# Optimization experiments

Hardware: AMD Instinct MI355X
Metric: run time of the kernel (lower is better)

## Reference

```python
import jax, jax.numpy as jnp
import numpy as np
import math

B, S, HID, HEADS = 4, 1024, 1024, 16
DH = HID // HEADS


def setup_inputs() -> dict:
    key = jax.random.key(0)
    ks = jax.random.split(key, 16)
    f = lambda k, shape: jax.random.normal(k, shape, dtype=jnp.float32)
    sc = 1.0 / math.sqrt(HID)
    return {
        "q_a": f(ks[0], (B, S, HID)), "k_a": f(ks[1], (B, S, HID)), "v_a": f(ks[2], (B, S, HID)),
        "q_b": f(ks[3], (B, S, HID)), "k_b": f(ks[4], (B, S, HID)), "v_b": f(ks[5], (B, S, HID)),
        "mask": jnp.ones((B, S), dtype=jnp.int32),
        "Wa": f(ks[6], (3, HID, HID)) * sc, "ba": jnp.zeros((3, HID), jnp.float32),
        "Wb": f(ks[7], (3, HID, HID)) * sc, "bb": jnp.zeros((3, HID), jnp.float32),
        "Wo_a": f(ks[8], (HID, HID)) * sc, "bo_a": jnp.zeros((HID,), jnp.float32),
        "Wo_b": f(ks[9], (HID, HID)) * sc, "bo_b": jnp.zeros((HID,), jnp.float32),
    }


def _proj(x, W, b):
    # torch Linear: x @ W.T + b, then split heads -> [B, heads, S, dh]
    y = x @ W.T + b
    return y.reshape(x.shape[0], -1, HEADS, DH).transpose(0, 2, 1, 3)


def reference(q_a, k_a, v_a, q_b, k_b, v_b, mask, Wa, ba, Wb, bb, Wo_a, bo_a, Wo_b, bo_b):
    qa, ka, va = _proj(q_a, Wa[0], ba[0]), _proj(k_a, Wa[1], ba[1]), _proj(v_a, Wa[2], ba[2])
    qb, kb, vb = _proj(q_b, Wb[0], bb[0]), _proj(k_b, Wb[1], bb[1]), _proj(v_b, Wb[2], bb[2])
    scale = 1.0 / math.sqrt(2 * DH)
    # dual-stream score fusion: self + cross terms, all scaled by 1/sqrt(2*dh)
    corr_a = (jnp.einsum('bhqd,bhkd->bhqk', qa, ka) + jnp.einsum('bhqd,bhkd->bhqk', qa, kb)) * scale
    corr_b = (jnp.einsum('bhqd,bhkd->bhqk', qb, kb) + jnp.einsum('bhqd,bhkd->bhqk', qb, ka)) * scale
    m = (mask == 0)[:, None, None, :]  # key-padding mask broadcast over heads & queries
    corr_a = jnp.where(m, -1e9, corr_a)
    corr_b = jnp.where(m, -1e9, corr_b)
    pa = jax.nn.softmax(corr_a, axis=-1)
    pb = jax.nn.softmax(corr_b, axis=-1)
    ha = jnp.einsum('bhqk,bhkd->bhqd', pa, va).transpose(0, 2, 1, 3).reshape(q_a.shape[0], -1, HID)
    hb = jnp.einsum('bhqk,bhkd->bhqd', pb, vb).transpose(0, 2, 1, 3).reshape(q_b.shape[0], -1, HID)
    return (ha @ Wo_a.T + bo_a, hb @ Wo_b.T + bo_b)
```

## Files before the change

### kernel.cpp

```cpp
#include <hip/hip_runtime.h>


typedef __bf16 bf16;
typedef __bf16 bf16x4 __attribute__((ext_vector_type(4)));
typedef __bf16 bf16x8 __attribute__((ext_vector_type(8)));
typedef float  f32x4  __attribute__((ext_vector_type(4)));

#define HID_C   1024
#define S_C     1024
#define B_C     4
#define H_C     16
#define DH_C    64
#define NTOK    4096

__device__ __forceinline__ void gl_lds16(const bf16* g, bf16* l) {
    __builtin_amdgcn_global_load_lds(
        (const __attribute__((address_space(1))) void*)g,
        (__attribute__((address_space(3))) void*)l, 16, 0, 0);
}

struct CvtArgs {
    const float* src[10];
    bf16*        dst[10];
    int          cum[11];
};

__global__ __launch_bounds__(256) void cvt_all(CvtArgs a) {
    int blk = blockIdx.x;
    int seg = 0;
    while (blk >= a.cum[seg + 1]) ++seg;
    int i = ((blk - a.cum[seg]) * 256 + threadIdx.x) * 4;
    f32x4 v = *(const f32x4*)(a.src[seg] + i);
    *(bf16x4*)(a.dst[seg] + i) = __builtin_convertvector(v, bf16x4);
}

struct GemmJob {
    const bf16* A1; const bf16* W1;
    const bf16* A2; const bf16* W2;
    const float* bias1; const float* bias2;
    void* out; int mode; float scale;
};
struct GemmBatch { GemmJob j[5]; };

__global__ __launch_bounds__(256, 3)
void gemm_bt(GemmBatch gb) {
    const GemmJob jb = gb.j[blockIdx.z];
    const int K = HID_C;
    __shared__ bf16 a_lds[128 * 64];
    __shared__ bf16 w_lds[128 * 64];

    const int tid  = threadIdx.x;
    const int wave = tid >> 6, lane = tid & 63;
    const int quad = lane >> 4, l15 = lane & 15;
    const int swz  = l15 & 7;
    const int row0 = blockIdx.x * 128;
    const int col0 = blockIdx.y * 128;
    const int wr = (wave >> 1) * 64;
    const int wc = (wave & 1) * 64;

    f32x4 acc[4][4] = {};

    const int nkb = jb.A2 ? 32 : 16;
    for (int kb = 0; kb < nkb; ++kb) {
        const bf16* A = (kb < 16) ? jb.A1 : jb.A2;
        const bf16* W = (kb < 16) ? jb.W1 : jb.W2;
        const int k0 = (kb & 15) * 64;
        __syncthreads();
        for (int i = 0; i < 4; ++i) {
            int q = tid + i * 256;
            int r = q >> 3, c = q & 7;
            int gch = c ^ (r & 7);
            gl_lds16(A + (size_t)(row0 + r) * K + k0 + gch * 8, a_lds + q * 8);
            gl_lds16(W + (size_t)(col0 + r) * K + k0 + gch * 8, w_lds + q * 8);
        }
        __syncthreads();
        for (int kk = 0; kk < 2; ++kk) {
            const int ch = ((kk * 4 + quad) ^ swz) * 8;
            bf16x8 af[4], bw[4];
            for (int mi = 0; mi < 4; ++mi)
                af[mi] = *(const bf16x8*)(a_lds + (wr + mi * 16 + l15) * 64 + ch);
            for (int ni = 0; ni < 4; ++ni)
                bw[ni] = *(const bf16x8*)(w_lds + (wc + ni * 16 + l15) * 64 + ch);
            for (int mi = 0; mi < 4; ++mi)
                for (int ni = 0; ni < 4; ++ni)
                    acc[mi][ni] = __builtin_amdgcn_mfma_f32_16x16x32_bf16(af[mi], bw[ni], acc[mi][ni], 0, 0, 0);
        }
    }

    for (int mi = 0; mi < 4; ++mi) {
        for (int ni = 0; ni < 4; ++ni) {
            int colg = col0 + wc + ni * 16 + l15;
            float bv = jb.bias1 ? jb.bias1[colg] : 0.f;
            if (jb.bias2) bv += jb.bias2[colg];
            for (int r = 0; r < 4; ++r) {
                int rowg = row0 + wr + mi * 16 + quad * 4 + r;
                float v = (acc[mi][ni][r] + bv) * jb.scale;
                if (jb.mode == 2) {
                    ((float*)jb.out)[(size_t)rowg * HID_C + colg] = v;
                } else {
                    int b = rowg >> 10, s = rowg & 1023;
                    int h = colg >> 6,  d = colg & 63;
                    size_t idx = (jb.mode == 0)
                        ? ((size_t)((b * H_C + h) * S_C + s) * DH_C + d)
                        : ((size_t)((b * H_C + h) * DH_C + d) * S_C + s);
                    ((bf16*)jb.out)[idx] = (bf16)v;
                }
            }
        }
    }
}

__global__ __launch_bounds__(256, 2)
void attn_fused(const bf16* __restrict__ qp_a, const bf16* __restrict__ qp_b,
                const bf16* __restrict__ ksp,
                const bf16* __restrict__ vT_a, const bf16* __restrict__ vT_b,
                const int* __restrict__ mask,
                bf16* __restrict__ ho_a, bf16* __restrict__ ho_b) {
    __shared__ bf16  k_lds[2][128 * 64];
    __shared__ bf16  vT_lds[2][64 * 128];
    __shared__ float madd[1024];
    __shared__ bf16  p_lds[4 * 32 * 40];

    const int tid  = threadIdx.x;
    const int wave = tid >> 6, lane = tid & 63;
    const int quad = lane >> 4, l15 = lane & 15;
    const int swz  = l15 & 7;
    const int bh = blockIdx.x;
    const int b  = bh >> 4, h = bh & 15;
    const int s0 = blockIdx.y * 128;
    const bf16* qp   = blockIdx.z ? qp_b : qp_a;
    const bf16* vTp  = blockIdx.z ? vT_b : vT_a;
    bf16*       hout = blockIdx.z ? ho_b : ho_a;

    {
        int4 mv = *(const int4*)(mask + b * S_C + tid * 4);
        f32x4 md;
        md[0] = mv.x ? 0.f : -1e9f;
        md[1] = mv.y ? 0.f : -1e9f;
        md[2] = mv.z ? 0.f : -1e9f;
        md[3] = mv.w ? 0.f : -1e9f;
        *(f32x4*)(madd + tid * 4) = md;
    }

    bf16x8 qf[2][2];
    for (int qt = 0; qt < 2; ++qt)
        for (int kk = 0; kk < 2; ++kk)
            qf[qt][kk] = *(const bf16x8*)(qp + ((size_t)bh * S_C + s0 + wave * 32 + qt * 16 + l15) * DH_C
                                          + kk * 32 + quad * 8);

    const bf16* kbase0 = ksp + (size_t)bh * S_C * DH_C;
    const bf16* vbase0 = vTp + (size_t)bh * DH_C * S_C;
    auto stage = [&](int kt, int buf) {
        const bf16* kb = kbase0 + kt * 128 * DH_C;
        const bf16* vb = vbase0 + kt * 128;
        for (int i = 0; i < 4; ++i) {
            int q = tid + i * 256;
            int r = q >> 3, c = q & 7;
            gl_lds16(kb + r * DH_C + ((c ^ (r & 7)) * 8), &k_lds[buf][q * 8]);
            int d = q >> 4, c16 = q & 15;
            gl_lds16(vb + (size_t)d * S_C + ((c16 ^ (d & 7)) * 8), &vT_lds[buf][q * 8]);
        }
    };

    float m_i[2] = {-1e30f, -1e30f}, l_i[2] = {0.f, 0.f};
    f32x4 Oacc[2][4] = {};
    bf16* pw = p_lds + wave * (32 * 40);

    stage(0, 0);
    for (int kt = 0; kt < 8; ++kt) {
        const int cur = kt & 1;
        __syncthreads();
        if (kt < 7) stage(kt + 1, 1 - cur);
        const bf16* kl = k_lds[cur];
        const bf16* vl = vT_lds[cur];

        f32x4 sacc[8][2] = {};
        for (int kk = 0; kk < 2; ++kk) {
            const int ch = ((kk * 4 + quad) ^ swz) * 8;
            for (int ct = 0; ct < 8; ++ct) {
                bf16x8 kf = *(const bf16x8*)(kl + (ct * 16 + l15) * 64 + ch);
                sacc[ct][0] = __builtin_amdgcn_mfma_f32_16x16x32_bf16(kf, qf[0][kk], sacc[ct][0], 0, 0, 0);
                sacc[ct][1] = __builtin_amdgcn_mfma_f32_16x16x32_bf16(kf, qf[1][kk], sacc[ct][1], 0, 0, 0);
            }
        }
        for (int ct = 0; ct < 8; ++ct) {
            f32x4 md = *(const f32x4*)(madd + kt * 128 + ct * 16 + quad * 4);
            for (int qt = 0; qt < 2; ++qt)
                for (int r = 0; r < 4; ++r)
                    sacc[ct][qt][r] += md[r];
        }
        float fac[2];
        for (int qt = 0; qt < 2; ++qt) {
            float tm = sacc[0][qt][0];
            for (int ct = 0; ct < 8; ++ct)
                for (int r = 0; r < 4; ++r) tm = fmaxf(tm, sacc[ct][qt][r]);
            tm = fmaxf(tm, __shfl_xor(tm, 16, 64));
            tm = fmaxf(tm, __shfl_xor(tm, 32, 64));
            float mn = fmaxf(m_i[qt], tm);
            fac[qt] = __builtin_amdgcn_exp2f(m_i[qt] - mn);
            m_i[qt] = mn;
            float ts = 0.f;
            for (int ct = 0; ct < 8; ++ct)
                for (int r = 0; r < 4; ++r) {
                    float p = __builtin_amdgcn_exp2f(sacc[ct][qt][r] - mn);
                    sacc[ct][qt][r] = p;
                    ts += p;
                }
            ts += __shfl_xor(ts, 16, 64);
            ts += __shfl_xor(ts, 32, 64);
            l_i[qt] = l_i[qt] * fac[qt] + ts;
            for (int dt = 0; dt < 4; ++dt)
                for (int r = 0; r < 4; ++r) Oacc[qt][dt][r] *= fac[qt];
        }
        for (int c = 0; c < 4; ++c) {
            for (int qt = 0; qt < 2; ++qt)
                for (int half = 0; half < 2; ++half) {
                    bf16x4 pv = __builtin_convertvector(sacc[2 * c + half][qt], bf16x4);
                    *(bf16x4*)(pw + (qt * 16 + l15) * 40 + half * 16 + quad * 4) = pv;
                }
            bf16x8 pf0 = *(const bf16x8*)(pw + l15 * 40 + quad * 8);
            bf16x8 pf1 = *(const bf16x8*)(pw + (16 + l15) * 40 + quad * 8);
            for (int dt = 0; dt < 4; ++dt) {
                bf16x8 vf = *(const bf16x8*)(vl + (dt * 16 + l15) * 128 + ((c * 4 + quad) ^ swz) * 8);
                Oacc[0][dt] = __builtin_amdgcn_mfma_f32_16x16x32_bf16(vf, pf0, Oacc[0][dt], 0, 0, 0);
                Oacc[1][dt] = __builtin_amdgcn_mfma_f32_16x16x32_bf16(vf, pf1, Oacc[1][dt], 0, 0, 0);
            }
        }
    }

    for (int qt = 0; qt < 2; ++qt) {
        float inv = 1.f / l_i[qt];
        int token = s0 + wave * 32 + qt * 16 + l15;
        for (int dt = 0; dt < 4; ++dt) {
            f32x4 o;
            for (int r = 0; r < 4; ++r) o[r] = Oacc[qt][dt][r] * inv;
            bf16x4 ob = __builtin_convertvector(o, bf16x4);
            *(bf16x4*)(hout + (size_t)(b * S_C + token) * HID_C + h * DH_C + dt * 16 + quad * 4) = ob;
        }
    }
}

extern "C" void kernel_launch(void* const* d_in, const int* in_sizes, int n_in,
                              void* d_out, int out_size, void* d_ws, size_t ws_size,
                              hipStream_t stream) {
    const float* q_a  = (const float*)d_in[0];
    const float* k_a  = (const float*)d_in[1];
    const float* v_a  = (const float*)d_in[2];
    const float* q_b  = (const float*)d_in[3];
    const float* k_b  = (const float*)d_in[4];
    const float* v_b  = (const float*)d_in[5];
    const int*   mask = (const int*)  d_in[6];
    const float* Wa   = (const float*)d_in[7];
    const float* ba   = (const float*)d_in[8];
    const float* Wb   = (const float*)d_in[9];
    const float* bb   = (const float*)d_in[10];
    const float* Wo_a = (const float*)d_in[11];
    const float* bo_a = (const float*)d_in[12];
    const float* Wo_b = (const float*)d_in[13];
    const float* bo_b = (const float*)d_in[14];
    float* out = (float*)d_out;

    constexpr size_t ACT = (size_t)NTOK * HID_C;
    constexpr size_t W3  = 3 * (size_t)HID_C * HID_C;
    constexpr size_t W1  = (size_t)HID_C * HID_C;
    const float SC2 = 0.08838834764831845f * 1.4426950408889634f;

    bf16* w = (bf16*)d_ws;
    bf16* bfa[6];
    for (int i = 0; i < 6; ++i) bfa[i] = w + (size_t)i * ACT;
    bf16* bfWa  = w + 6 * ACT;
    bf16* bfWb  = bfWa + W3;
    bf16* bfWoA = bfWb + W3;
    bf16* bfWoB = bfWoA + W1;
    bf16* qa_p  = bfWoB + W1;
    bf16* qb_p  = qa_p + ACT;
    bf16* ks_p  = qb_p + ACT;
    bf16* vTa   = ks_p + ACT;
    bf16* vTb   = vTa + ACT;
    bf16* ha    = vTb + ACT;
    bf16* hb    = ha + ACT;

    CvtArgs ca;
    const float* srcs[10] = {q_a, k_a, v_a, q_b, k_b, v_b, Wa, Wb, Wo_a, Wo_b};
    bf16* dsts[10] = {bfa[0], bfa[1], bfa[2], bfa[3], bfa[4], bfa[5], bfWa, bfWb, bfWoA, bfWoB};
    int nblk[10] = {4096, 4096, 4096, 4096, 4096, 4096, 3072, 3072, 1024, 1024};
    int cum = 0;
    for (int i = 0; i < 10; ++i) { ca.src[i] = srcs[i]; ca.dst[i] = dsts[i]; ca.cum[i] = cum; cum += nblk[i]; }
    ca.cum[10] = cum;
    cvt_all<<<cum, 256, 0, stream>>>(ca);

    GemmBatch g1;
    g1.j[0] = { bfa[1], bfWa + W1,     bfa[4], bfWb + W1, ba + 1024, bb + 1024, ks_p, 0, 1.f  };
    g1.j[1] = { bfa[0], bfWa,          nullptr, nullptr,  ba,        nullptr,   qa_p, 0, SC2 };
    g1.j[2] = { bfa[3], bfWb,          nullptr, nullptr,  bb,        nullptr,   qb_p, 0, SC2 };
    g1.j[3] = { bfa[2], bfWa + 2 * W1, nullptr, nullptr,  ba + 2048, nullptr,   vTa,  1, 1.f  };
    g1.j[4] = { bfa[5], bfWb + 2 * W1, nullptr, nullptr,  bb + 2048, nullptr,   vTb,  1, 1.f  };
    gemm_bt<<<dim3(NTOK / 128, HID_C / 128, 5), 256, 0, stream>>>(g1);

    dim3 ga(B_C * H_C, S_C / 128, 2);
    attn_fused<<<ga, 256, 0, stream>>>(qa_p, qb_p, ks_p, vTa, vTb, mask, ha, hb);

    GemmBatch g2;
    g2.j[0] = { ha, bfWoA, nullptr, nullptr, bo_a, nullptr, (void*)out, 2, 1.f };
    g2.j[1] = { hb, bfWoB, nullptr, nullptr, bo_b, nullptr,
                (void*)(out + (size_t)NTOK * HID_C), 2, 1.f };
    g2.j[2] = g2.j[0]; g2.j[3] = g2.j[0]; g2.j[4] = g2.j[0];
    gemm_bt<<<dim3(NTOK / 128, HID_C / 128, 2), 256, 0, stream>>>(g2);
}
```

Before: 345.6 us.

## Process both attention streams per block to share K tiles; raise GEMM occupancy hint

The attention kernel now handles streams a and b in the same block, so each shared K tile is loaded into LDS once and used for both streams' scores. This halves the grid and removes the z dimension. The V loads are no longer double-buffered: they are issued at the start of each iteration, and two extra barriers per tile are added. Register pressure rises (two sets of Q fragments, accumulators and P tiles), which could lower occupancy or cause spills. Separately, the GEMM launch bound changes from 3 to 4 blocks per CU, which may force the compiler to use fewer registers.

```diff
diff --git a/kernel.cpp b/kernel.cpp
--- a/kernel.cpp
+++ b/kernel.cpp
@@ -42,7 +42,7 @@
 };
 struct GemmBatch { GemmJob j[5]; };
 
-__global__ __launch_bounds__(256, 3)
+__global__ __launch_bounds__(256, 4)
 void gemm_bt(GemmBatch gb) {
     const GemmJob jb = gb.j[blockIdx.z];
     const int K = HID_C;
@@ -117,7 +117,7 @@
                 const int* __restrict__ mask,
                 bf16* __restrict__ ho_a, bf16* __restrict__ ho_b) {
     __shared__ bf16  k_lds[2][128 * 64];
-    __shared__ bf16  vT_lds[2][64 * 128];
+    __shared__ bf16  v_lds[2][64 * 128];
     __shared__ float madd[1024];
     __shared__ bf16  p_lds[4 * 32 * 40];
 
@@ -128,9 +128,10 @@
     const int bh = blockIdx.x;
     const int b  = bh >> 4, h = bh & 15;
     const int s0 = blockIdx.y * 128;
-    const bf16* qp   = blockIdx.z ? qp_b : qp_a;
-    const bf16* vTp  = blockIdx.z ? vT_b : vT_a;
-    bf16*       hout = blockIdx.z ? ho_b : ho_a;
+
+    const bf16* qs[2] = {qp_a, qp_b};
+    const bf16* vs[2] = {vT_a, vT_b};
+    bf16*       hs[2] = {ho_a, ho_b};
 
     {
         int4 mv = *(const int4*)(mask + b * S_C + tid * 4);
@@ -142,102 +143,125 @@
         *(f32x4*)(madd + tid * 4) = md;
     }
 
-    bf16x8 qf[2][2];
-    for (int qt = 0; qt < 2; ++qt)
-        for (int kk = 0; kk < 2; ++kk)
-            qf[qt][kk] = *(const bf16x8*)(qp + ((size_t)bh * S_C + s0 + wave * 32 + qt * 16 + l15) * DH_C
-                                          + kk * 32 + quad * 8);
+    bf16x8 qf[2][2][2];
+    for (int st = 0; st < 2; ++st)
+        for (int qt = 0; qt < 2; ++qt)
+            for (int kk = 0; kk < 2; ++kk)
+                qf[st][qt][kk] = *(const bf16x8*)(qs[st]
+                    + ((size_t)bh * S_C + s0 + wave * 32 + qt * 16 + l15) * DH_C
+                    + kk * 32 + quad * 8);
 
     const bf16* kbase0 = ksp + (size_t)bh * S_C * DH_C;
-    const bf16* vbase0 = vTp + (size_t)bh * DH_C * S_C;
-    auto stage = [&](int kt, int buf) {
-        const bf16* kb = kbase0 + kt * 128 * DH_C;
-        const bf16* vb = vbase0 + kt * 128;
-        for (int i = 0; i < 4; ++i) {
-            int q = tid + i * 256;
-            int r = q >> 3, c = q & 7;
-            gl_lds16(kb + r * DH_C + ((c ^ (r & 7)) * 8), &k_lds[buf][q * 8]);
-            int d = q >> 4, c16 = q & 15;
-            gl_lds16(vb + (size_t)d * S_C + ((c16 ^ (d & 7)) * 8), &vT_lds[buf][q * 8]);
-        }
-    };
-
-    float m_i[2] = {-1e30f, -1e30f}, l_i[2] = {0.f, 0.f};
-    f32x4 Oacc[2][4] = {};
+
+    float m_i[2][2], l_i[2][2];
+    for (int st = 0; st < 2; ++st)
+        for (int qt = 0; qt < 2; ++qt) { m_i[st][qt] = -1e30f; l_i[st][qt] = 0.f; }
+    f32x4  Oacc[2][2][4] = {};
+    bf16x4 pk[2][8][2];
     bf16* pw = p_lds + wave * (32 * 40);
 
-    stage(0, 0);
+    for (int i = 0; i < 4; ++i) {
+        int q = tid + i * 256;
+        int r = q >> 3, c = q & 7;
+        gl_lds16(kbase0 + r * DH_C + ((c ^ (r & 7)) * 8), &k_lds[0][q * 8]);
+    }
+    __syncthreads();
+
     for (int kt = 0; kt < 8; ++kt) {
         const int cur = kt & 1;
+        for (int st = 0; st < 2; ++st) {
+            const bf16* vb = vs[st] + (size_t)bh * DH_C * S_C + kt * 128;
+            for (int i = 0; i < 4; ++i) {
+                int q = tid + i * 256;
+                int d = q >> 4, c16 = q & 15;
+                gl_lds16(vb + (size_t)d * S_C + ((c16 ^ (d & 7)) * 8), &v_lds[st][q * 8]);
+            }
+        }
+        if (kt < 7) {
+            const bf16* kb = kbase0 + (kt + 1) * 128 * DH_C;
+            for (int i = 0; i < 4; ++i) {
+                int q = tid + i * 256;
+                int r = q >> 3, c = q & 7;
+                gl_lds16(kb + r * DH_C + ((c ^ (r & 7)) * 8), &k_lds[1 - cur][q * 8]);
+            }
+        }
+        const bf16* kl = k_lds[cur];
+
+        for (int st = 0; st < 2; ++st) {
+            f32x4 sacc[8][2] = {};
+            for (int kk = 0; kk < 2; ++kk) {
+                const int ch = ((kk * 4 + quad) ^ swz) * 8;
+                for (int ct = 0; ct < 8; ++ct) {
+                    bf16x8 kf = *(const bf16x8*)(kl + (ct * 16 + l15) * 64 + ch);
+                    sacc[ct][0] = __builtin_amdgcn_mfma_f32_16x16x32_bf16(kf, qf[st][0][kk], sacc[ct][0], 0, 0, 0);
+                    sacc[ct][1] = __builtin_amdgcn_mfma_f32_16x16x32_bf16(kf, qf[st][1][kk], sacc[ct][1], 0, 0, 0);
+                }
+            }
+            for (int ct = 0; ct < 8; ++ct) {
+                f32x4 md = *(const f32x4*)(madd + kt * 128 + ct * 16 + quad * 4);
+                for (int qt = 0; qt < 2; ++qt)
+                    for (int r = 0; r < 4; ++r)
+                        sacc[ct][qt][r] += md[r];
+            }
+            for (int qt = 0; qt < 2; ++qt) {
+                float tm = sacc[0][qt][0];
+                for (int ct = 0; ct < 8; ++ct)
+                    for (int r = 0; r < 4; ++r) tm = fmaxf(tm, sacc[ct][qt][r]);
+                tm = fmaxf(tm, __shfl_xor(tm, 16, 64));
+                tm = fmaxf(tm, __shfl_xor(tm, 32, 64));
+                float mn = fmaxf(m_i[st][qt], tm);
+                float fac = __builtin_amdgcn_exp2f(m_i[st][qt] - mn);
+                m_i[st][qt] = mn;
+                float ts = 0.f;
+                for (int ct = 0; ct < 8; ++ct)
+                    for (int r = 0; r < 4; ++r) {
+                        float p = __builtin_amdgcn_exp2f(sacc[ct][qt][r] - mn);
+                        sacc[ct][qt][r] = p;
+                        ts += p;
+                    }
+                ts += __shfl_xor(ts, 16, 64);
+                ts += __shfl_xor(ts, 32, 64);
+                l_i[st][qt] = l_i[st][qt] * fac + ts;
+                for (int dt = 0; dt < 4; ++dt)
+                    for (int r = 0; r < 4; ++r) Oacc[st][qt][dt][r] *= fac;
+                for (int ct = 0; ct < 8; ++ct)
+                    pk[st][ct][qt] = __builtin_convertvector(sacc[ct][qt], bf16x4);
+            }
+        }
+
         __syncthreads();
-        if (kt < 7) stage(kt + 1, 1 - cur);
-        const bf16* kl = k_lds[cur];
-        const bf16* vl = vT_lds[cur];
-
-        f32x4 sacc[8][2] = {};
-        for (int kk = 0; kk < 2; ++kk) {
-            const int ch = ((kk * 4 + quad) ^ swz) * 8;
-            for (int ct = 0; ct < 8; ++ct) {
-                bf16x8 kf = *(const bf16x8*)(kl + (ct * 16 + l15) * 64 + ch);
-                sacc[ct][0] = __builtin_amdgcn_mfma_f32_16x16x32_bf16(kf, qf[0][kk], sacc[ct][0], 0, 0, 0);
-                sacc[ct][1] = __builtin_amdgcn_mfma_f32_16x16x32_bf16(kf, qf[1][kk], sacc[ct][1], 0, 0, 0);
-            }
-        }
-        for (int ct = 0; ct < 8; ++ct) {
-            f32x4 md = *(const f32x4*)(madd + kt * 128 + ct * 16 + quad * 4);
-            for (int qt = 0; qt < 2; ++qt)
-                for (int r = 0; r < 4; ++r)
-                    sacc[ct][qt][r] += md[r];
-        }
-        float fac[2];
+
+        for (int st = 0; st < 2; ++st) {
+            const bf16* vl = v_lds[st];
+            for (int c = 0; c < 4; ++c) {
+                for (int qt = 0; qt < 2; ++qt)
+                    for (int half = 0; half < 2; ++half)
+                        *(bf16x4*)(pw + (qt * 16 + l15) * 40 + half * 16 + quad * 4)
+                            = pk[st][2 * c + half][qt];
+                bf16x8 pf0 = *(const bf16x8*)(pw + l15 * 40 + quad * 8);
+                bf16x8 pf1 = *(const bf16x8*)(pw + (16 + l15) * 40 + quad * 8);
+                for (int dt = 0; dt < 4; ++dt) {
+                    bf16x8 vf = *(const bf16x8*)(vl + (dt * 16 + l15) * 128 + ((c * 4 + quad) ^ swz) * 8);
+                    Oacc[st][0][dt] = __builtin_amdgcn_mfma_f32_16x16x32_bf16(vf, pf0, Oacc[st][0][dt], 0, 0, 0);
+                    Oacc[st][1][dt] = __builtin_amdgcn_mfma_f32_16x16x32_bf16(vf, pf1, Oacc[st][1][dt], 0, 0, 0);
+                }
+            }
+        }
+
+        __syncthreads();
+    }
+
+    for (int st = 0; st < 2; ++st)
         for (int qt = 0; qt < 2; ++qt) {
-            float tm = sacc[0][qt][0];
-            for (int ct = 0; ct < 8; ++ct)
-                for (int r = 0; r < 4; ++r) tm = fmaxf(tm, sacc[ct][qt][r]);
-            tm = fmaxf(tm, __shfl_xor(tm, 16, 64));
-            tm = fmaxf(tm, __shfl_xor(tm, 32, 64));
-            float mn = fmaxf(m_i[qt], tm);
-            fac[qt] = __builtin_amdgcn_exp2f(m_i[qt] - mn);
-            m_i[qt] = mn;
-            float ts = 0.f;
-            for (int ct = 0; ct < 8; ++ct)
-                for (int r = 0; r < 4; ++r) {
-                    float p = __builtin_amdgcn_exp2f(sacc[ct][qt][r] - mn);
-                    sacc[ct][qt][r] = p;
-                    ts += p;
-                }
-            ts += __shfl_xor(ts, 16, 64);
-            ts += __shfl_xor(ts, 32, 64);
-            l_i[qt] = l_i[qt] * fac[qt] + ts;
-            for (int dt = 0; dt < 4; ++dt)
-                for (int r = 0; r < 4; ++r) Oacc[qt][dt][r] *= fac[qt];
-        }
-        for (int c = 0; c < 4; ++c) {
-            for (int qt = 0; qt < 2; ++qt)
-                for (int half = 0; half < 2; ++half) {
-                    bf16x4 pv = __builtin_convertvector(sacc[2 * c + half][qt], bf16x4);
-                    *(bf16x4*)(pw + (qt * 16 + l15) * 40 + half * 16 + quad * 4) = pv;
-                }
-            bf16x8 pf0 = *(const bf16x8*)(pw + l15 * 40 + quad * 8);
-            bf16x8 pf1 = *(const bf16x8*)(pw + (16 + l15) * 40 + quad * 8);
+            float inv = 1.f / l_i[st][qt];
+            int token = s0 + wave * 32 + qt * 16 + l15;
             for (int dt = 0; dt < 4; ++dt) {
-                bf16x8 vf = *(const bf16x8*)(vl + (dt * 16 + l15) * 128 + ((c * 4 + quad) ^ swz) * 8);
-                Oacc[0][dt] = __builtin_amdgcn_mfma_f32_16x16x32_bf16(vf, pf0, Oacc[0][dt], 0, 0, 0);
-                Oacc[1][dt] = __builtin_amdgcn_mfma_f32_16x16x32_bf16(vf, pf1, Oacc[1][dt], 0, 0, 0);
-            }
-        }
-    }
-
-    for (int qt = 0; qt < 2; ++qt) {
-        float inv = 1.f / l_i[qt];
-        int token = s0 + wave * 32 + qt * 16 + l15;
-        for (int dt = 0; dt < 4; ++dt) {
-            f32x4 o;
-            for (int r = 0; r < 4; ++r) o[r] = Oacc[qt][dt][r] * inv;
-            bf16x4 ob = __builtin_convertvector(o, bf16x4);
-            *(bf16x4*)(hout + (size_t)(b * S_C + token) * HID_C + h * DH_C + dt * 16 + quad * 4) = ob;
-        }
-    }
+                f32x4 o;
+                for (int r = 0; r < 4; ++r) o[r] = Oacc[st][qt][dt][r] * inv;
+                bf16x4 ob = __builtin_convertvector(o, bf16x4);
+                *(bf16x4*)(hs[st] + (size_t)(b * S_C + token) * HID_C + h * DH_C + dt * 16 + quad * 4) = ob;
+            }
+        }
 }
 
 extern "C" void kernel_launch(void* const* d_in, const int* in_sizes, int n_in,
@@ -297,7 +321,7 @@
     g1.j[4] = { bfa[5], bfWb + 2 * W1, nullptr, nullptr,  bb + 2048, nullptr,   vTb,  1, 1.f  };
     gemm_bt<<<dim3(NTOK / 128, HID_C / 128, 5), 256, 0, stream>>>(g1);
 
-    dim3 ga(B_C * H_C, S_C / 128, 2);
+    dim3 ga(B_C * H_C, S_C / 128);
     attn_fused<<<ga, 256, 0, stream>>>(qa_p, qb_p, ks_p, vTa, vTb, mask, ha, hb);
 
     GemmBatch g2;
```

Measured after the change: 374.9 us. 1.08x slower.
